# Performance work log

Hardware: AMD Instinct MI355X
Metric: run time of the kernel (lower is better)

Reference implementation:

```python
import jax, jax.numpy as jnp
import numpy as np

N = 4096
INPUT_SIZE = 1024
HIDDEN = 512


def setup_inputs() -> dict:
    key = jax.random.key(0)
    ks = jax.random.split(key, 7)
    s_in = 1.0 / np.sqrt(INPUT_SIZE)
    return {
        "embs": jax.random.normal(ks[0], (N, INPUT_SIZE), dtype=jnp.float32),
        "Wq": jax.random.uniform(ks[1], (HIDDEN, INPUT_SIZE), jnp.float32, -s_in, s_in),
        "bq": jax.random.uniform(ks[2], (HIDDEN,), jnp.float32, -s_in, s_in),
        "Wk": jax.random.uniform(ks[3], (HIDDEN, INPUT_SIZE), jnp.float32, -s_in, s_in),
        "bk": jax.random.uniform(ks[4], (HIDDEN,), jnp.float32, -s_in, s_in),
        "Wv": jax.random.uniform(ks[5], (HIDDEN, INPUT_SIZE), jnp.float32, -s_in, s_in),
        "bv": jax.random.uniform(ks[6], (HIDDEN,), jnp.float32, -s_in, s_in),
    }


def reference(embs, Wq, bq, Wk, bk, Wv, bv):
    # Linear projections (nn.Linear: x @ W.T + b)
    q = embs @ Wq.T + bq   # [N, H]
    k = embs @ Wk.T + bk   # [N, H]
    v = embs @ Wv.T + bv   # [N, H]
    # Unscaled attention scores, softmax over keys (dim=1)
    scores = jax.nn.softmax(q @ k.T, axis=1)  # [N, N]
    # Per-query weighted sum over values == scores @ v
    return scores @ v  # [N, H]
```

## Files before the change

kernel.cpp:

```cpp
#include <hip/hip_runtime.h>
#include <stdint.h>

#define NT 4096
#define DI 1024
#define DH 512

typedef _Float16 f16;
typedef _Float16 half8 __attribute__((ext_vector_type(8)));
typedef short short8 __attribute__((ext_vector_type(8)));
typedef float f32x4 __attribute__((ext_vector_type(4)));
typedef short s16;

__device__ __forceinline__ s16 to_bf16(float f) {
  uint32_t u = __builtin_bit_cast(uint32_t, f);
  u += 0x7FFFu + ((u >> 16) & 1u);
  return (s16)(u >> 16);
}
__device__ __forceinline__ float from_bf16(s16 s) {
  uint32_t u = ((uint32_t)(uint16_t)s) << 16;
  return __builtin_bit_cast(float, u);
}

__device__ __forceinline__ void gload_lds16(const void* g, void* l) {
  void* gnc = const_cast<void*>(g);
  __builtin_amdgcn_global_load_lds(
      (__attribute__((address_space(1))) void*)gnc,
      (__attribute__((address_space(3))) void*)l,
      16, 0, 0);
}

__global__ __launch_bounds__(256)
void cvt_all(const float4* __restrict__ e,  const float4* __restrict__ wq,
             const float4* __restrict__ wk, const float4* __restrict__ wv,
             half8* __restrict__ de, half8* __restrict__ dq,
             half8* __restrict__ dk, half8* __restrict__ dv) {
  int b = blockIdx.x;
  const float4* src; half8* dst; int i;
  if (b < 2048)      { src = e;  dst = de; i = b * 256 + threadIdx.x; }
  else if (b < 2304) { src = wq; dst = dq; i = (b - 2048) * 256 + threadIdx.x; }
  else if (b < 2560) { src = wk; dst = dk; i = (b - 2304) * 256 + threadIdx.x; }
  else               { src = wv; dst = dv; i = (b - 2560) * 256 + threadIdx.x; }
  float4 a = src[2 * i], c = src[2 * i + 1];
  half8 h;
  h[0] = (f16)a.x; h[1] = (f16)a.y; h[2] = (f16)a.z; h[3] = (f16)a.w;
  h[4] = (f16)c.x; h[5] = (f16)c.y; h[6] = (f16)c.z; h[7] = (f16)c.w;
  dst[i] = h;
}

template<int MODE>
__global__ __launch_bounds__(256)
void gemm_bt(const s16* __restrict__ A, const s16* __restrict__ B0,
             s16* __restrict__ O16,
             s16* __restrict__ oq, s16* __restrict__ ok, s16* __restrict__ ovT,
             const float* __restrict__ bq, const float* __restrict__ bk,
             const float* __restrict__ bv,
             float* __restrict__ Daux,
             int M, int Nn, int K, int lda, int ldb, int ldc)
{
  __shared__ __align__(16) s16 At[2][128 * 32];
  __shared__ __align__(16) s16 Bt[2][128 * 32];

  const int tid  = threadIdx.x;
  const int lane = tid & 63;
  const int wave = tid >> 6;
  const int wr = wave >> 1, wc = wave & 1;

  int bxi = blockIdx.x, byi = blockIdx.y, kchunk = 0;
  if (MODE == 2) {
    int bid = blockIdx.x;
    kchunk = bid & 7;
    bxi = (bid >> 3) & 3;
    byi = bid >> 5;
  }
  const int bm = byi * 128;
  const int bn = bxi * 128;

  const s16* Bmat = B0;
  const float* bias = nullptr;
  if (MODE == 1) {
    int z = blockIdx.z;
    Bmat = B0 + (size_t)z * DH * DI;
    bias = (z == 0) ? bq : (z == 1) ? bk : bv;
  }
  if (MODE == 2) {
    int koff = kchunk * K;
    A    += koff;
    Bmat  = B0 + koff;
  }

  const int frow = lane & 15;
  const int kslc = (lane >> 4) * 8;

  f32x4 acc[4][4];
#pragma unroll
  for (int i = 0; i < 4; ++i)
#pragma unroll
    for (int j = 0; j < 4; ++j) acc[i][j] = (f32x4){0.f, 0.f, 0.f, 0.f};

  float rsum[4] = {0.f, 0.f, 0.f, 0.f};

  const int nk = K >> 5;

  auto stage = [&](int buf, int kt) {
#pragma unroll
    for (int cc = 0; cc < 2; ++cc) {
      int c  = wave * 2 + cc;
      int e8 = c * 64 + lane;
      int r  = e8 >> 2;
      int c8 = e8 & 3;
      gload_lds16(A    + (size_t)(bm + r) * lda + kt * 32 + c8 * 8, &At[buf][c * 512]);
      gload_lds16(Bmat + (size_t)(bn + r) * ldb + kt * 32 + c8 * 8, &Bt[buf][c * 512]);
    }
  };

  stage(0, 0);
  __syncthreads();

  for (int kt = 0; kt < nk; ++kt) {
    const int cur = kt & 1;
    if (kt + 1 < nk) stage(cur ^ 1, kt + 1);
    short8 af[4], bf[4];
#pragma unroll
    for (int mi = 0; mi < 4; ++mi)
      af[mi] = *(const short8*)&At[cur][(wr * 64 + mi * 16 + frow) * 32 + kslc];
#pragma unroll
    for (int ni = 0; ni < 4; ++ni)
      bf[ni] = *(const short8*)&Bt[cur][(wc * 64 + ni * 16 + frow) * 32 + kslc];

    if (MODE == 2) {
#pragma unroll
      for (int mi = 0; mi < 4; ++mi)
#pragma unroll
        for (int j = 0; j < 8; ++j) rsum[mi] += from_bf16(af[mi][j]);
    }

#pragma unroll
    for (int mi = 0; mi < 4; ++mi)
#pragma unroll
      for (int ni = 0; ni < 4; ++ni) {
        if (MODE == 2)
          acc[mi][ni] = __builtin_amdgcn_mfma_f32_16x16x32_bf16(af[mi], bf[ni], acc[mi][ni], 0, 0, 0);
        else
          acc[mi][ni] = __builtin_amdgcn_mfma_f32_16x16x32_f16(
              __builtin_bit_cast(half8, af[mi]), __builtin_bit_cast(half8, bf[ni]),
              acc[mi][ni], 0, 0, 0);
      }
    __syncthreads();
  }

  if (MODE == 2) {
#pragma unroll
    for (int mi = 0; mi < 4; ++mi) {
      float s = rsum[mi];
      s += __shfl_xor(s, 16);
      s += __shfl_xor(s, 32);
      if ((wave & 1) == 0 && lane < 16)
        Daux[(size_t)kchunk * NT + bm + wr * 64 + mi * 16 + lane] = s;
    }
  }

  const int rbase = (lane >> 4) * 4;
#pragma unroll
  for (int mi = 0; mi < 4; ++mi) {
#pragma unroll
    for (int ni = 0; ni < 4; ++ni) {
#pragma unroll
      for (int j = 0; j < 4; ++j) {
        int gr = bm + wr * 64 + mi * 16 + rbase + j;
        int gc = bn + wc * 64 + ni * 16 + frow;
        float v = acc[mi][ni][j];
        if (MODE == 1) {
          v += bias[gc];
          int z = blockIdx.z;
          if (z == 0)      oq[(size_t)gr * ldc + gc] = __builtin_bit_cast(s16, (f16)v);
          else if (z == 1) ok[(size_t)gr * ldc + gc] = __builtin_bit_cast(s16, (f16)v);
          else             ovT[(size_t)gc * M + gr] = to_bf16(v);
        } else if (MODE == 2) {
          O16[(size_t)kchunk * NT * DH + (size_t)gr * DH + gc] = to_bf16(v);
        } else {
          O16[(size_t)gr * ldc + gc] = to_bf16(__expf(fminf(v - 45.f, 80.f)));
        }
      }
    }
  }
}

__global__ __launch_bounds__(256)
void combine_pv(const s16* __restrict__ Np, const float* __restrict__ Dp,
                float* __restrict__ out) {
  int gi = blockIdx.x * 256 + threadIdx.x;
  int r  = gi >> 6;
  int d8 = (gi & 63) * 8;
  float D = 0.f;
#pragma unroll
  for (int c = 0; c < 8; ++c) D += Dp[c * NT + r];
  float a[8];
#pragma unroll
  for (int j = 0; j < 8; ++j) a[j] = 0.f;
#pragma unroll
  for (int c = 0; c < 8; ++c) {
    short8 h = *(const short8*)&Np[(size_t)c * NT * DH + (size_t)r * DH + d8];
#pragma unroll
    for (int j = 0; j < 8; ++j) a[j] += from_bf16(h[j]);
  }
  float inv = 1.f / D;
  float4* o4 = (float4*)&out[(size_t)r * DH + d8];
  o4[0] = (float4){a[0] * inv, a[1] * inv, a[2] * inv, a[3] * inv};
  o4[1] = (float4){a[4] * inv, a[5] * inv, a[6] * inv, a[7] * inv};
}

extern "C" void kernel_launch(void* const* d_in, const int* in_sizes, int n_in,
                              void* d_out, int out_size, void* d_ws, size_t ws_size,
                              hipStream_t stream) {
  const float* embs = (const float*)d_in[0];
  const float* Wq   = (const float*)d_in[1];
  const float* bq   = (const float*)d_in[2];
  const float* Wk   = (const float*)d_in[3];
  const float* bk   = (const float*)d_in[4];
  const float* Wv   = (const float*)d_in[5];
  const float* bv   = (const float*)d_in[6];
  float* out = (float*)d_out;

  char* ws = (char*)d_ws;
  s16*   P      = (s16*)(ws);
  s16*   embs16 = (s16*)(ws);
  s16*   W16    = (s16*)(ws + 8388608);
  s16*   Npart  = (s16*)(ws + 33554432);
  float* Dpart  = (float*)(ws + 67108864);
  s16*   q16    = (s16*)(ws + 67239936);
  s16*   k16    = (s16*)(ws + 71434240);
  s16*   vT16   = (s16*)(ws + 75628544);

  cvt_all<<<2816, 256, 0, stream>>>(
      (const float4*)embs, (const float4*)Wq, (const float4*)Wk, (const float4*)Wv,
      (half8*)embs16, (half8*)W16, (half8*)(W16 + 524288), (half8*)(W16 + 1048576));

  gemm_bt<1><<<dim3(4, 32, 3), 256, 0, stream>>>(
      embs16, W16, nullptr, q16, k16, vT16, bq, bk, bv, nullptr,
      4096, 512, 1024, 1024, 1024, 512);

  gemm_bt<0><<<dim3(32, 32, 1), 256, 0, stream>>>(
      q16, k16, P, nullptr, nullptr, nullptr, nullptr, nullptr, nullptr, nullptr,
      4096, 4096, 512, 512, 512, 4096);

  gemm_bt<2><<<dim3(1024, 1, 1), 256, 0, stream>>>(
      P, vT16, Npart, nullptr, nullptr, nullptr, nullptr, nullptr, nullptr, Dpart,
      4096, 512, 512, 4096, 4096, 512);

  combine_pv<<<1024, 256, 0, stream>>>(Npart, Dpart, out);
}
```

Measured before the change: 176.5 us.

## Compute softmax denominators in QK^T epilogue with atomics instead of PV row sums

Moves the softmax row-sum computation out of the PV GEMM main loop, where it summed bf16 A fragments every K step, into the QK^T GEMM epilogue. There the fp32 exp values are reduced with warp shuffles and accumulated per row with global atomicAdd. An extra block in the conversion kernel zeroes the denominator buffer, and the combine kernel reads one value per row. This removes VALU work from the PV inner loop. In exchange it adds many atomics in the score kernel, and the denominator now comes from unrounded fp32 values, so it no longer exactly matches the bf16 values used in the numerator.

Result: slower. 185.7 us (+5.2%).

```diff
diff --git a/kernel.cpp b/kernel.cpp
--- a/kernel.cpp
+++ b/kernel.cpp
@@ -33,8 +33,16 @@
 void cvt_all(const float4* __restrict__ e,  const float4* __restrict__ wq,
              const float4* __restrict__ wk, const float4* __restrict__ wv,
              half8* __restrict__ de, half8* __restrict__ dq,
-             half8* __restrict__ dk, half8* __restrict__ dv) {
+             half8* __restrict__ dk, half8* __restrict__ dv,
+             float* __restrict__ Dz) {
   int b = blockIdx.x;
+  if (b == 2816) {
+    float4 z = (float4){0.f, 0.f, 0.f, 0.f};
+    float4* D4 = (float4*)Dz;
+#pragma unroll
+    for (int j = 0; j < 4; ++j) D4[threadIdx.x * 4 + j] = z;
+    return;
+  }
   const float4* src; half8* dst; int i;
   if (b < 2048)      { src = e;  dst = de; i = b * 256 + threadIdx.x; }
   else if (b < 2304) { src = wq; dst = dq; i = (b - 2048) * 256 + threadIdx.x; }
@@ -97,8 +105,6 @@
 #pragma unroll
     for (int j = 0; j < 4; ++j) acc[i][j] = (f32x4){0.f, 0.f, 0.f, 0.f};
 
-  float rsum[4] = {0.f, 0.f, 0.f, 0.f};
-
   const int nk = K >> 5;
 
   auto stage = [&](int buf, int kt) {
@@ -126,14 +132,6 @@
 #pragma unroll
     for (int ni = 0; ni < 4; ++ni)
       bf[ni] = *(const short8*)&Bt[cur][(wc * 64 + ni * 16 + frow) * 32 + kslc];
-
-    if (MODE == 2) {
-#pragma unroll
-      for (int mi = 0; mi < 4; ++mi)
-#pragma unroll
-        for (int j = 0; j < 8; ++j) rsum[mi] += from_bf16(af[mi][j]);
-    }
-
 #pragma unroll
     for (int mi = 0; mi < 4; ++mi)
 #pragma unroll
@@ -148,25 +146,15 @@
     __syncthreads();
   }
 
-  if (MODE == 2) {
-#pragma unroll
-    for (int mi = 0; mi < 4; ++mi) {
-      float s = rsum[mi];
-      s += __shfl_xor(s, 16);
-      s += __shfl_xor(s, 32);
-      if ((wave & 1) == 0 && lane < 16)
-        Daux[(size_t)kchunk * NT + bm + wr * 64 + mi * 16 + lane] = s;
-    }
-  }
-
   const int rbase = (lane >> 4) * 4;
 #pragma unroll
   for (int mi = 0; mi < 4; ++mi) {
 #pragma unroll
-    for (int ni = 0; ni < 4; ++ni) {
-#pragma unroll
-      for (int j = 0; j < 4; ++j) {
-        int gr = bm + wr * 64 + mi * 16 + rbase + j;
+    for (int j = 0; j < 4; ++j) {
+      int gr = bm + wr * 64 + mi * 16 + rbase + j;
+      float s4 = 0.f;
+#pragma unroll
+      for (int ni = 0; ni < 4; ++ni) {
         int gc = bn + wc * 64 + ni * 16 + frow;
         float v = acc[mi][ni][j];
         if (MODE == 1) {
@@ -178,22 +166,28 @@
         } else if (MODE == 2) {
           O16[(size_t)kchunk * NT * DH + (size_t)gr * DH + gc] = to_bf16(v);
         } else {
-          O16[(size_t)gr * ldc + gc] = to_bf16(__expf(fminf(v - 45.f, 80.f)));
+          float p = __expf(fminf(v - 45.f, 80.f));
+          s4 += p;
+          O16[(size_t)gr * ldc + gc] = to_bf16(p);
         }
       }
+      if (MODE == 0) {
+        s4 += __shfl_xor(s4, 1);
+        s4 += __shfl_xor(s4, 2);
+        s4 += __shfl_xor(s4, 4);
+        s4 += __shfl_xor(s4, 8);
+        if (frow == 0) atomicAdd(&Daux[gr], s4);
+      }
     }
   }
 }
 
 __global__ __launch_bounds__(256)
-void combine_pv(const s16* __restrict__ Np, const float* __restrict__ Dp,
+void combine_pv(const s16* __restrict__ Np, const float* __restrict__ Dfull,
                 float* __restrict__ out) {
   int gi = blockIdx.x * 256 + threadIdx.x;
   int r  = gi >> 6;
   int d8 = (gi & 63) * 8;
-  float D = 0.f;
-#pragma unroll
-  for (int c = 0; c < 8; ++c) D += Dp[c * NT + r];
   float a[8];
 #pragma unroll
   for (int j = 0; j < 8; ++j) a[j] = 0.f;
@@ -203,7 +197,7 @@
 #pragma unroll
     for (int j = 0; j < 8; ++j) a[j] += from_bf16(h[j]);
   }
-  float inv = 1.f / D;
+  float inv = 1.f / Dfull[r];
   float4* o4 = (float4*)&out[(size_t)r * DH + d8];
   o4[0] = (float4){a[0] * inv, a[1] * inv, a[2] * inv, a[3] * inv};
   o4[1] = (float4){a[4] * inv, a[5] * inv, a[6] * inv, a[7] * inv};
@@ -226,26 +220,27 @@
   s16*   embs16 = (s16*)(ws);
   s16*   W16    = (s16*)(ws + 8388608);
   s16*   Npart  = (s16*)(ws + 33554432);
-  float* Dpart  = (float*)(ws + 67108864);
+  float* Dfull  = (float*)(ws + 67108864);
   s16*   q16    = (s16*)(ws + 67239936);
   s16*   k16    = (s16*)(ws + 71434240);
   s16*   vT16   = (s16*)(ws + 75628544);
 
-  cvt_all<<<2816, 256, 0, stream>>>(
+  cvt_all<<<2817, 256, 0, stream>>>(
       (const float4*)embs, (const float4*)Wq, (const float4*)Wk, (const float4*)Wv,
-      (half8*)embs16, (half8*)W16, (half8*)(W16 + 524288), (half8*)(W16 + 1048576));
+      (half8*)embs16, (half8*)W16, (half8*)(W16 + 524288), (half8*)(W16 + 1048576),
+      Dfull);
 
   gemm_bt<1><<<dim3(4, 32, 3), 256, 0, stream>>>(
       embs16, W16, nullptr, q16, k16, vT16, bq, bk, bv, nullptr,
       4096, 512, 1024, 1024, 1024, 512);
 
   gemm_bt<0><<<dim3(32, 32, 1), 256, 0, stream>>>(
-      q16, k16, P, nullptr, nullptr, nullptr, nullptr, nullptr, nullptr, nullptr,
+      q16, k16, P, nullptr, nullptr, nullptr, nullptr, nullptr, nullptr, Dfull,
       4096, 4096, 512, 512, 512, 4096);
 
   gemm_bt<2><<<dim3(1024, 1, 1), 256, 0, stream>>>(
-      P, vT16, Npart, nullptr, nullptr, nullptr, nullptr, nullptr, nullptr, Dpart,
+      P, vT16, Npart, nullptr, nullptr, nullptr, nullptr, nullptr, nullptr, nullptr,
       4096, 512, 512, 4096, 4096, 512);
 
-  combine_pv<<<1024, 256, 0, stream>>>(Npart, Dpart, out);
-}
+  combine_pv<<<1024, 256, 0, stream>>>(Npart, Dfull, out);
+}
```
